# Performance work log

Hardware: AMD Instinct MI355X
Metric: run time of the kernel (lower is better)

Reference implementation:

```python
import jax, jax.numpy as jnp
from jax import lax
import numpy as np

B, T, EPROJS, DUNITS, ATT_DIM = 32, 2048, 1024, 1024, 1024
ACONV_CHANS, ACONV_FILTS = 10, 100
SCALING = 2.0


def setup_inputs() -> dict:
    key = jax.random.key(0)
    ks = jax.random.split(key, 12)
    s = 0.02
    return {
        "enc_hs_pad": jax.random.normal(ks[0], (B, T, EPROJS), jnp.float32),
        "enc_hs_len": jax.random.randint(ks[1], (B,), T // 2, T + 1, jnp.int32),
        "dec_z": jax.random.normal(ks[2], (B, DUNITS), jnp.float32),
        "att_prev": jax.random.uniform(ks[3], (B, T), jnp.float32) / T,
        "W_enc": jax.random.normal(ks[4], (EPROJS, ATT_DIM), jnp.float32) * s,
        "b_enc": jnp.zeros((ATT_DIM,), jnp.float32),
        "W_dec": jax.random.normal(ks[5], (DUNITS, ATT_DIM), jnp.float32) * s,
        "W_att": jax.random.normal(ks[6], (ACONV_CHANS, ATT_DIM), jnp.float32) * s,
        "conv_w": jax.random.normal(ks[7], (ACONV_CHANS, 1, 2 * ACONV_FILTS + 1), jnp.float32) * s,
        "gvec_w": jax.random.normal(ks[8], (ATT_DIM,), jnp.float32) * s,
        "gvec_b": jnp.zeros((), jnp.float32),
    }


def reference(enc_hs_pad, enc_hs_len, dec_z, att_prev, W_enc, b_enc, W_dec, W_att, conv_w, gvec_w, gvec_b):
    # location conv over previous attention: (B,1,T) -> (B,C,T), 'same' padding
    pad = (conv_w.shape[-1] - 1) // 2
    att_conv = lax.conv_general_dilated(
        att_prev[:, None, :], conv_w, window_strides=(1,),
        padding=[(pad, pad)], dimension_numbers=("NCH", "OIH", "NCH"))  # (B,C,T)
    loc = jnp.einsum("bct,cd->btd", att_conv, W_att)                     # mlp_att
    enc_proj = jnp.einsum("bte,ed->btd", enc_hs_pad, W_enc) + b_enc      # pre_compute_enc_h
    dec_proj = (dec_z @ W_dec)[:, None, :]                               # (B,1,D)
    e = jnp.tanh(loc + enc_proj + dec_proj) @ gvec_w + gvec_b            # (B,T)
    mask = jnp.arange(T)[None, :] >= enc_hs_len[:, None]                 # pad mask
    e = jnp.where(mask, -jnp.inf, e)
    w = jax.nn.softmax(SCALING * e, axis=1)                              # (B,T)
    c = jnp.einsum("bt,bte->be", w, enc_hs_pad)                          # weighted sum
    return c, w
```

## Files before the change

### kernel.cpp

```cpp
#include <hip/hip_runtime.h>
#include <hip/hip_bf16.h>
#include <math.h>

#define BB 32
#define TT 2048
#define EE 1024
#define DD 1024
#define MM (BB * TT)
#define CC 10
#define FW 201

typedef __attribute__((ext_vector_type(8))) short short8;
typedef __attribute__((ext_vector_type(4))) float f32x4;
typedef __attribute__((ext_vector_type(4))) float f4;
typedef __attribute__((ext_vector_type(8))) unsigned short u16x8;
typedef unsigned short u16;

__device__ __forceinline__ u16 f2bf(float f) {
  __hip_bfloat16 h = __float2bfloat16(f);
  return *reinterpret_cast<u16*>(&h);
}
__device__ __forceinline__ float bf2f(u16 u) {
  __hip_bfloat16 h;
  *reinterpret_cast<u16*>(&h) = u;
  return __bfloat162float(h);
}

__global__ void k_zero(float* __restrict__ e, float* __restrict__ c) {
  int i = blockIdx.x * 256 + threadIdx.x;
  e[i] = 0.f;
  if (i < BB * DD) c[i] = 0.f;
}

__global__ void k_cvt(const float* __restrict__ enc, u16* __restrict__ out) {
  long i = (long)blockIdx.x * 256 + threadIdx.x;
  const f4* ep = (const f4*)enc;
  f4 x = ep[2 * i], y = ep[2 * i + 1];
  u16x8 o;
  o[0] = f2bf(x[0]); o[1] = f2bf(x[1]); o[2] = f2bf(x[2]); o[3] = f2bf(x[3]);
  o[4] = f2bf(y[0]); o[5] = f2bf(y[1]); o[6] = f2bf(y[2]); o[7] = f2bf(y[3]);
  ((u16x8*)out)[i] = o;
}

__global__ void k_tw(const float* __restrict__ W, u16* __restrict__ Wt) {
  __shared__ float tile[64][65];
  int k0 = (blockIdx.x & 15) * 64;
  int n0 = (blockIdx.x >> 4) * 64;
  int tid = threadIdx.x;
  for (int i = tid; i < 4096; i += 256) {
    int r = i >> 6, cc = i & 63;
    tile[r][cc] = W[(k0 + r) * 1024 + n0 + cc];
  }
  __syncthreads();
  for (int i = tid; i < 4096; i += 256) {
    int nr = i >> 6, kc = i & 63;
    Wt[(n0 + nr) * 1024 + k0 + kc] = f2bf(tile[kc][nr]);
  }
}

__global__ void k_conv(const float* __restrict__ att_prev, const float* __restrict__ conv_w,
                       float* __restrict__ attc) {
  __shared__ float cw[CC * FW];
  __shared__ float ap[256 + 2 * 100];
  int b = blockIdx.x >> 3;
  int t0 = (blockIdx.x & 7) * 256;
  int tid = threadIdx.x;
  for (int i = tid; i < CC * FW; i += 256) cw[i] = conv_w[i];
  for (int i = tid; i < 456; i += 256) {
    int t = t0 - 100 + i;
    ap[i] = (t >= 0 && t < TT) ? att_prev[b * TT + t] : 0.f;
  }
  __syncthreads();
  float acc[CC];
#pragma unroll
  for (int c = 0; c < CC; ++c) acc[c] = 0.f;
  for (int f = 0; f < FW; ++f) {
    float x = ap[tid + f];
#pragma unroll
    for (int c = 0; c < CC; ++c) acc[c] += x * cw[c * FW + f];
  }
  int t = t0 + tid;
  float* o = attc + (size_t)(b * TT + t) * CC;
#pragma unroll
  for (int c = 0; c < CC; ++c) o[c] = acc[c];
}

__global__ void k_decp(const float* __restrict__ dec_z, const float* __restrict__ W_dec,
                       float* __restrict__ decp) {
  int b = blockIdx.x >> 2, dc = blockIdx.x & 3;
  __shared__ float z[1024];
  for (int i = threadIdx.x; i < 1024; i += 256) z[i] = dec_z[(b << 10) + i];
  __syncthreads();
  int d = (dc << 8) + threadIdx.x;
  float a0 = 0, a1 = 0, a2 = 0, a3 = 0;
  for (int k = 0; k < 1024; k += 4) {
    a0 += z[k + 0] * W_dec[(k + 0) * 1024 + d];
    a1 += z[k + 1] * W_dec[(k + 1) * 1024 + d];
    a2 += z[k + 2] * W_dec[(k + 2) * 1024 + d];
    a3 += z[k + 3] * W_dec[(k + 3) * 1024 + d];
  }
  decp[(b << 10) + d] = (a0 + a1) + (a2 + a3);
}

__global__ __launch_bounds__(256, 2) void k_gemm(
    const u16* __restrict__ A, const u16* __restrict__ Bt,
    const float* __restrict__ benc, const float* __restrict__ decp,
    const float* __restrict__ attc, const float* __restrict__ watt,
    const float* __restrict__ gvec, float* __restrict__ e) {
  __shared__ u16 sA[2][128 * 32];
  __shared__ u16 sB[2][128 * 32];
  __shared__ float s_col[128];
  __shared__ float s_g[128];
  __shared__ float s_watt[CC * 128];
  __shared__ float s_attc[128 * CC];
  __shared__ float s_ep[128][2];

  int tid = threadIdx.x;
  int w = tid >> 6, lane = tid & 63;
  int orig = ((blockIdx.x & 7) << 9) + (blockIdx.x >> 3);
  int bm = orig >> 3, bn = orig & 7;
  int brow = bm << 7;
  int bcol = bn << 7;
  int b = brow >> 11;

  if (tid < 128) {
    s_col[tid] = benc[bcol + tid] + decp[(b << 10) + bcol + tid];
    s_g[tid] = gvec[bcol + tid];
    s_ep[tid][0] = 0.f;
    s_ep[tid][1] = 0.f;
  }
  for (int i = tid; i < CC * 128; i += 256) {
    int c = i >> 7, d = i & 127;
    s_watt[c * 128 + d] = watt[c * 1024 + bcol + d];
  }
  for (int i = tid; i < 128 * CC; i += 256)
    s_attc[i] = attc[(size_t)brow * CC + i];

  f32x4 acc[4][4];
#pragma unroll
  for (int i = 0; i < 4; ++i)
#pragma unroll
    for (int j = 0; j < 4; ++j) acc[i][j] = (f32x4){0.f, 0.f, 0.f, 0.f};

  int wm = w >> 1, wn = w & 1;
  int frl = lane & 15, fkg = lane >> 4;

  auto stage = [&](int buf, int kt) {
    int k0 = kt << 5;
#pragma unroll
    for (int q = 0; q < 2; ++q) {
      int ci = (q << 8) + (w << 6) + lane;
      int row = ci >> 2, p = ci & 3;
      int kg = (p - (row >> 1)) & 3;
      const u16* ga = A + (size_t)(brow + row) * 1024 + k0 + (kg << 3);
      u16* la = &sA[buf][((q << 8) + (w << 6)) << 3];
      __builtin_amdgcn_global_load_lds(
          (const __attribute__((address_space(1))) void*)ga,
          (__attribute__((address_space(3))) void*)la, 16, 0, 0);
      const u16* gb = Bt + (size_t)(bcol + row) * 1024 + k0 + (kg << 3);
      u16* lb = &sB[buf][((q << 8) + (w << 6)) << 3];
      __builtin_amdgcn_global_load_lds(
          (const __attribute__((address_space(1))) void*)gb,
          (__attribute__((address_space(3))) void*)lb, 16, 0, 0);
    }
  };

  stage(0, 0);
  __syncthreads();

  for (int kt = 0; kt < 32; ++kt) {
    int cur = kt & 1;
    if (kt < 31) stage(cur ^ 1, kt + 1);
    short8 af[4], bfr[4];
#pragma unroll
    for (int mi = 0; mi < 4; ++mi) {
      int r = (wm << 6) + (mi << 4) + frl;
      int p = (fkg + (r >> 1)) & 3;
      af[mi] = *(const short8*)&sA[cur][(r << 5) + (p << 3)];
    }
#pragma unroll
    for (int ni = 0; ni < 4; ++ni) {
      int r = (wn << 6) + (ni << 4) + frl;
      int p = (fkg + (r >> 1)) & 3;
      bfr[ni] = *(const short8*)&sB[cur][(r << 5) + (p << 3)];
    }
#pragma unroll
    for (int mi = 0; mi < 4; ++mi)
#pragma unroll
      for (int ni = 0; ni < 4; ++ni)
        acc[mi][ni] = __builtin_amdgcn_mfma_f32_16x16x32_bf16(af[mi], bfr[ni], acc[mi][ni], 0, 0, 0);
    __syncthreads();
  }

#pragma unroll
  for (int mi = 0; mi < 4; ++mi) {
#pragma unroll
    for (int j = 0; j < 4; ++j) {
      int rl = (wm << 6) + (mi << 4) + (fkg << 2) + j;
      float ar[CC];
#pragma unroll
      for (int c = 0; c < CC; ++c) ar[c] = s_attc[rl * CC + c];
      float esum = 0.f;
#pragma unroll
      for (int ni = 0; ni < 4; ++ni) {
        int col = (wn << 6) + (ni << 4) + frl;
        float qv = acc[mi][ni][j] + s_col[col];
#pragma unroll
        for (int c = 0; c < CC; ++c) qv += ar[c] * s_watt[c * 128 + col];
        esum += s_g[col] * tanhf(qv);
      }
#pragma unroll
      for (int o = 8; o >= 1; o >>= 1) esum += __shfl_xor(esum, o, 16);
      if (frl == 0) s_ep[rl][wn] = esum;
    }
  }
  __syncthreads();
  if (tid < 128) atomicAdd(&e[brow + tid], s_ep[tid][0] + s_ep[tid][1]);
}

__global__ __launch_bounds__(256) void k_softmax(const float* __restrict__ e,
                                                 const int* __restrict__ len,
                                                 float* __restrict__ wout) {
  int b = blockIdx.x;
  int L = len[b];
  const float* eb = e + b * TT;
  __shared__ float red[4], red2[4];
  int tid = threadIdx.x, w = tid >> 6, lane = tid & 63;
  float m = -3.4e38f;
  for (int t = tid; t < TT; t += 256)
    if (t < L) m = fmaxf(m, eb[t]);
  for (int o = 32; o >= 1; o >>= 1) m = fmaxf(m, __shfl_xor(m, o, 64));
  if (lane == 0) red[w] = m;
  __syncthreads();
  m = fmaxf(fmaxf(red[0], red[1]), fmaxf(red[2], red[3]));
  float s = 0.f;
  for (int t = tid; t < TT; t += 256)
    if (t < L) s += __expf(2.f * (eb[t] - m));
  for (int o = 32; o >= 1; o >>= 1) s += __shfl_xor(s, o, 64);
  if (lane == 0) red2[w] = s;
  __syncthreads();
  s = red2[0] + red2[1] + red2[2] + red2[3];
  float inv = 1.f / s;
  for (int t = tid; t < TT; t += 256)
    wout[b * TT + t] = (t < L) ? __expf(2.f * (eb[t] - m)) * inv : 0.f;
}

__global__ __launch_bounds__(256) void k_ctx(const u16* __restrict__ encbf,
                                             const float* __restrict__ wout,
                                             float* __restrict__ c) {
  int bid = blockIdx.x;
  int b = bid >> 5;
  int ec = (bid >> 3) & 3;
  int tc = bid & 7;
  int col = (ec << 8) + threadIdx.x;
  const u16* eb = encbf + ((size_t)(b * TT + tc * 256) << 10) + col;
  const float* wb = wout + b * TT + tc * 256;
  float a0 = 0, a1 = 0, a2 = 0, a3 = 0;
  for (int t = 0; t < 256; t += 4) {
    a0 += wb[t + 0] * bf2f(eb[(size_t)(t + 0) << 10]);
    a1 += wb[t + 1] * bf2f(eb[(size_t)(t + 1) << 10]);
    a2 += wb[t + 2] * bf2f(eb[(size_t)(t + 2) << 10]);
    a3 += wb[t + 3] * bf2f(eb[(size_t)(t + 3) << 10]);
  }
  atomicAdd(&c[(b << 10) + col], (a0 + a1) + (a2 + a3));
}

extern "C" void kernel_launch(void* const* d_in, const int* in_sizes, int n_in,
                              void* d_out, int out_size, void* d_ws, size_t ws_size,
                              hipStream_t stream) {
  const float* enc = (const float*)d_in[0];
  const int* elen = (const int*)d_in[1];
  const float* dec_z = (const float*)d_in[2];
  const float* att_prev = (const float*)d_in[3];
  const float* W_enc = (const float*)d_in[4];
  const float* b_enc = (const float*)d_in[5];
  const float* W_dec = (const float*)d_in[6];
  const float* W_att = (const float*)d_in[7];
  const float* conv_w = (const float*)d_in[8];
  const float* gvec_w = (const float*)d_in[9];

  char* ws = (char*)d_ws;
  u16* encbf = (u16*)ws;  ws += (size_t)MM * EE * 2;
  u16* Wt = (u16*)ws;     ws += (size_t)EE * DD * 2;
  float* attc = (float*)ws; ws += (size_t)MM * CC * 4;
  float* decp = (float*)ws; ws += (size_t)BB * DD * 4;
  float* e = (float*)ws;    ws += (size_t)MM * 4;

  float* c = (float*)d_out;
  float* wout = c + BB * DD;

  k_zero<<<256, 256, 0, stream>>>(e, c);
  k_cvt<<<(MM * EE / 8) / 256, 256, 0, stream>>>(enc, encbf);
  k_tw<<<256, 256, 0, stream>>>(W_enc, Wt);
  k_conv<<<256, 256, 0, stream>>>(att_prev, conv_w, attc);
  k_decp<<<128, 256, 0, stream>>>(dec_z, W_dec, decp);
  k_gemm<<<4096, 256, 0, stream>>>(encbf, Wt, b_enc, decp, attc, W_att, gvec_w, e);
  k_softmax<<<BB, 256, 0, stream>>>(e, elen, wout);
  k_ctx<<<1024, 256, 0, stream>>>(encbf, wout, c);
}
```

Before: 732.5 us.

## Rewrite attention GEMM with 256x256 tiles, deep LDS pipeline, and vectorized context

The main GEMM moves from 128x128 tiles with 256 threads to 256x256 tiles with 512 threads and 128KB of dynamic LDS. Its K loop is a multi-stage global_load_lds pipeline with explicit vmcnt waits, barriers and setprio around the MFMA bursts. Per-column partial energies are written to four separate buffers and summed in softmax, so the atomics and the zeroing pass for e go away. tanhf is replaced by an exp/rcp approximation. The decoder projection is split along K across more blocks, and the context kernel uses 8-wide bf16 loads and skips zero weights. The larger tiles cut operand refetch, at the cost of higher register and LDS pressure, which could limit occupancy.

Measured after the change: 715.1 us. 1.02x faster.

```diff
diff --git a/kernel.cpp b/kernel.cpp
--- a/kernel.cpp
+++ b/kernel.cpp
@@ -25,11 +25,14 @@
   *reinterpret_cast<u16*>(&h) = u;
   return __bfloat162float(h);
 }
-
-__global__ void k_zero(float* __restrict__ e, float* __restrict__ c) {
+__device__ __forceinline__ float tanh_fast(float x) {
+  float ex = __expf(2.f * x);
+  return 1.f - 2.f * __builtin_amdgcn_rcpf(ex + 1.f);
+}
+
+__global__ void k_zero(float* __restrict__ c) {
   int i = blockIdx.x * 256 + threadIdx.x;
-  e[i] = 0.f;
-  if (i < BB * DD) c[i] = 0.f;
+  c[i] = 0.f;
 }
 
 __global__ void k_cvt(const float* __restrict__ enc, u16* __restrict__ out) {
@@ -85,184 +88,253 @@
   for (int c = 0; c < CC; ++c) o[c] = acc[c];
 }
 
-__global__ void k_decp(const float* __restrict__ dec_z, const float* __restrict__ W_dec,
-                       float* __restrict__ decp) {
-  int b = blockIdx.x >> 2, dc = blockIdx.x & 3;
+__global__ __launch_bounds__(256) void k_decp(const float* __restrict__ dec_z,
+                                              const float* __restrict__ W_dec,
+                                              float* __restrict__ decp) {
+  int b = blockIdx.x >> 4;
+  int c0 = (blockIdx.x & 15) << 6;
   __shared__ float z[1024];
+  __shared__ float red[4][64];
   for (int i = threadIdx.x; i < 1024; i += 256) z[i] = dec_z[(b << 10) + i];
   __syncthreads();
-  int d = (dc << 8) + threadIdx.x;
-  float a0 = 0, a1 = 0, a2 = 0, a3 = 0;
-  for (int k = 0; k < 1024; k += 4) {
-    a0 += z[k + 0] * W_dec[(k + 0) * 1024 + d];
-    a1 += z[k + 1] * W_dec[(k + 1) * 1024 + d];
-    a2 += z[k + 2] * W_dec[(k + 2) * 1024 + d];
-    a3 += z[k + 3] * W_dec[(k + 3) * 1024 + d];
-  }
-  decp[(b << 10) + d] = (a0 + a1) + (a2 + a3);
-}
-
-__global__ __launch_bounds__(256, 2) void k_gemm(
+  int d = c0 + (threadIdx.x & 63), ks = threadIdx.x >> 6;
+  float a = 0.f;
+  const float* Wp = W_dec + (size_t)(ks << 8) * 1024 + d;
+  const float* zp = z + (ks << 8);
+#pragma unroll 4
+  for (int k = 0; k < 256; ++k) a += zp[k] * Wp[(size_t)k * 1024];
+  red[ks][threadIdx.x & 63] = a;
+  __syncthreads();
+  if (threadIdx.x < 64)
+    decp[(b << 10) + c0 + threadIdx.x] =
+        (red[0][threadIdx.x] + red[1][threadIdx.x]) + (red[2][threadIdx.x] + red[3][threadIdx.x]);
+}
+
+#define VM8 asm volatile("s_waitcnt vmcnt(8)" ::: "memory")
+#define VM4 asm volatile("s_waitcnt vmcnt(4)" ::: "memory")
+#define VM0 asm volatile("s_waitcnt vmcnt(0)" ::: "memory")
+
+__global__ __launch_bounds__(512, 2) void k_gemm8(
     const u16* __restrict__ A, const u16* __restrict__ Bt,
     const float* __restrict__ benc, const float* __restrict__ decp,
     const float* __restrict__ attc, const float* __restrict__ watt,
-    const float* __restrict__ gvec, float* __restrict__ e) {
-  __shared__ u16 sA[2][128 * 32];
-  __shared__ u16 sB[2][128 * 32];
-  __shared__ float s_col[128];
-  __shared__ float s_g[128];
-  __shared__ float s_watt[CC * 128];
-  __shared__ float s_attc[128 * CC];
-  __shared__ float s_ep[128][2];
+    const float* __restrict__ gvec, float* __restrict__ epart) {
+  extern __shared__ u16 smem[];
+  u16* sA = smem;
+  u16* sB = smem + 32768;
 
   int tid = threadIdx.x;
-  int w = tid >> 6, lane = tid & 63;
-  int orig = ((blockIdx.x & 7) << 9) + (blockIdx.x >> 3);
-  int bm = orig >> 3, bn = orig & 7;
-  int brow = bm << 7;
-  int bcol = bn << 7;
+  int lane = tid & 63, wid = tid >> 6;
+  int frl = lane & 15, fkg = lane >> 4;
+  int wm = wid >> 2, wn = wid & 3;
+
+  int orig = (blockIdx.x & 7) * 128 + (blockIdx.x >> 3);
+  int bm = orig >> 2, bn = orig & 3;
+  int brow = bm << 8;
+  int bcol = bn << 8;
   int b = brow >> 11;
 
-  if (tid < 128) {
-    s_col[tid] = benc[bcol + tid] + decp[(b << 10) + bcol + tid];
-    s_g[tid] = gvec[bcol + tid];
-    s_ep[tid][0] = 0.f;
-    s_ep[tid][1] = 0.f;
-  }
-  for (int i = tid; i < CC * 128; i += 256) {
-    int c = i >> 7, d = i & 127;
-    s_watt[c * 128 + d] = watt[c * 1024 + bcol + d];
-  }
-  for (int i = tid; i < 128 * CC; i += 256)
-    s_attc[i] = attc[(size_t)brow * CC + i];
-
-  f32x4 acc[4][4];
-#pragma unroll
-  for (int i = 0; i < 4; ++i)
-#pragma unroll
-    for (int j = 0; j < 4; ++j) acc[i][j] = (f32x4){0.f, 0.f, 0.f, 0.f};
-
-  int wm = w >> 1, wn = w & 1;
-  int frl = lane & 15, fkg = lane >> 4;
-
-  auto stage = [&](int buf, int kt) {
-    int k0 = kt << 5;
+  auto stA = [&](int par, int kk, int tile) {
+    u16* region = sA + ((par * 2 + kk) << 13);
+    const u16* gb = A + (size_t)brow * 1024 + tile * 64 + kk * 32;
 #pragma unroll
     for (int q = 0; q < 2; ++q) {
-      int ci = (q << 8) + (w << 6) + lane;
-      int row = ci >> 2, p = ci & 3;
-      int kg = (p - (row >> 1)) & 3;
-      const u16* ga = A + (size_t)(brow + row) * 1024 + k0 + (kg << 3);
-      u16* la = &sA[buf][((q << 8) + (w << 6)) << 3];
+      int s = (q << 9) + tid;
+      int r = s >> 2, ch = s & 3;
+      int cs = ch ^ ((r >> 1) & 3);
+      const u16* src = gb + (size_t)r * 1024 + (cs << 3);
+      u16* dst = region + (((q << 9) + (tid & ~63)) << 3);
       __builtin_amdgcn_global_load_lds(
-          (const __attribute__((address_space(1))) void*)ga,
-          (__attribute__((address_space(3))) void*)la, 16, 0, 0);
-      const u16* gb = Bt + (size_t)(bcol + row) * 1024 + k0 + (kg << 3);
-      u16* lb = &sB[buf][((q << 8) + (w << 6)) << 3];
-      __builtin_amdgcn_global_load_lds(
-          (const __attribute__((address_space(1))) void*)gb,
-          (__attribute__((address_space(3))) void*)lb, 16, 0, 0);
+          (const __attribute__((address_space(1))) void*)src,
+          (__attribute__((address_space(3))) void*)dst, 16, 0, 0);
     }
   };
-
-  stage(0, 0);
-  __syncthreads();
-
-  for (int kt = 0; kt < 32; ++kt) {
-    int cur = kt & 1;
-    if (kt < 31) stage(cur ^ 1, kt + 1);
-    short8 af[4], bfr[4];
-#pragma unroll
-    for (int mi = 0; mi < 4; ++mi) {
-      int r = (wm << 6) + (mi << 4) + frl;
-      int p = (fkg + (r >> 1)) & 3;
-      af[mi] = *(const short8*)&sA[cur][(r << 5) + (p << 3)];
+  auto stB = [&](int par, int kk, int tile) {
+    u16* region = sB + ((par * 2 + kk) << 13);
+    const u16* gb = Bt + (size_t)bcol * 1024 + tile * 64 + kk * 32;
+#pragma unroll
+    for (int q = 0; q < 2; ++q) {
+      int s = (q << 9) + tid;
+      int r = s >> 2, ch = s & 3;
+      int cs = ch ^ ((r >> 1) & 3);
+      const u16* src = gb + (size_t)r * 1024 + (cs << 3);
+      u16* dst = region + (((q << 9) + (tid & ~63)) << 3);
+      __builtin_amdgcn_global_load_lds(
+          (const __attribute__((address_space(1))) void*)src,
+          (__attribute__((address_space(3))) void*)dst, 16, 0, 0);
     }
-#pragma unroll
-    for (int ni = 0; ni < 4; ++ni) {
-      int r = (wn << 6) + (ni << 4) + frl;
-      int p = (fkg + (r >> 1)) & 3;
-      bfr[ni] = *(const short8*)&sB[cur][(r << 5) + (p << 3)];
+  };
+  auto rdA = [&](int par, int kk, int mi) -> short8 {
+    int row = (wm << 7) + (mi << 4) + frl;
+    int g = fkg ^ ((row >> 1) & 3);
+    return *(const short8*)(sA + ((par * 2 + kk) << 13) + (row << 5) + (g << 3));
+  };
+  auto rdB = [&](int par, int kk, int ni) -> short8 {
+    int row = (wn << 6) + (ni << 4) + frl;
+    int g = fkg ^ ((row >> 1) & 3);
+    return *(const short8*)(sB + ((par * 2 + kk) << 13) + (row << 5) + (g << 3));
+  };
+
+  f32x4 acc[8][4];
+#pragma unroll
+  for (int i = 0; i < 8; ++i)
+#pragma unroll
+    for (int j = 0; j < 4; ++j) acc[i][j] = (f32x4){0.f, 0.f, 0.f, 0.f};
+  short8 afr[4], bfr[4];
+
+#define PH(PAR, KK, CH, STAGE, WAIT)                                          \
+  {                                                                           \
+    if ((CH) == 0) {                                                          \
+      _Pragma("unroll") for (int ni = 0; ni < 4; ++ni)                        \
+          bfr[ni] = rdB(PAR, KK, ni);                                         \
+    }                                                                         \
+    _Pragma("unroll") for (int i = 0; i < 4; ++i)                             \
+        afr[i] = rdA(PAR, KK, (CH)*4 + i);                                    \
+    STAGE;                                                                    \
+    WAIT;                                                                     \
+    __builtin_amdgcn_s_barrier();                                             \
+    __builtin_amdgcn_s_setprio(1);                                            \
+    _Pragma("unroll") for (int i = 0; i < 4; ++i)                             \
+        _Pragma("unroll") for (int ni = 0; ni < 4; ++ni)                      \
+            acc[(CH)*4 + i][ni] = __builtin_amdgcn_mfma_f32_16x16x32_bf16(    \
+                afr[i], bfr[ni], acc[(CH)*4 + i][ni], 0, 0, 0);               \
+    __builtin_amdgcn_s_setprio(0);                                            \
+    __builtin_amdgcn_s_barrier();                                             \
+  }
+
+  stA(0, 0, 0); stB(0, 0, 0);
+  stA(0, 1, 0); stB(0, 1, 0);
+  stA(1, 0, 1); stB(1, 0, 1);
+  VM8;
+  __builtin_amdgcn_s_barrier();
+
+#pragma unroll 1
+  for (int I = 0; I < 7; ++I) {
+    int t = 2 * I;
+    PH(0, 0, 0, stA(1, 1, t + 1), ((void)0));
+    PH(0, 0, 1, stB(1, 1, t + 1), VM8);
+    PH(0, 1, 0, stA(0, 0, t + 2), ((void)0));
+    PH(0, 1, 1, stB(0, 0, t + 2), VM8);
+    PH(1, 0, 0, stA(0, 1, t + 2), ((void)0));
+    PH(1, 0, 1, stB(0, 1, t + 2), VM8);
+    PH(1, 1, 0, stA(1, 0, t + 3), ((void)0));
+    PH(1, 1, 1, stB(1, 0, t + 3), VM8);
+  }
+  PH(0, 0, 0, stA(1, 1, 15), ((void)0));
+  PH(0, 0, 1, stB(1, 1, 15), VM8);
+  PH(0, 1, 0, ((void)0), ((void)0));
+  PH(0, 1, 1, ((void)0), VM4);
+  PH(1, 0, 0, ((void)0), ((void)0));
+  PH(1, 0, 1, ((void)0), VM0);
+  PH(1, 1, 0, ((void)0), ((void)0));
+  PH(1, 1, 1, ((void)0), ((void)0));
+#undef PH
+
+  __syncthreads();
+  float* fsm = (float*)smem;
+  float* se_attc = fsm;
+  float* se_watt = fsm + 2560;
+  float* se_col  = fsm + 5120;
+  float* se_g    = fsm + 5376;
+  float* se_ep   = fsm + 5632;
+  for (int i = tid; i < 2560; i += 512) {
+    se_attc[i] = attc[(size_t)brow * 10 + i];
+    se_watt[i] = watt[(i >> 8) * 1024 + bcol + (i & 255)];
+  }
+  if (tid < 256) {
+    se_col[tid] = benc[bcol + tid] + decp[(b << 10) + bcol + tid];
+    se_g[tid] = gvec[bcol + tid];
+  }
+  __syncthreads();
+
+#pragma unroll
+  for (int mi = 0; mi < 8; ++mi) {
+#pragma unroll
+    for (int j = 0; j < 4; ++j) {
+      int rl = (wm << 7) + (mi << 4) + (fkg << 2) + j;
+      float ar[CC];
+#pragma unroll
+      for (int c = 0; c < CC; ++c) ar[c] = se_attc[rl * 10 + c];
+      float esum = 0.f;
+#pragma unroll
+      for (int ni = 0; ni < 4; ++ni) {
+        int cl = (wn << 6) + (ni << 4) + frl;
+        float qv = acc[mi][ni][j] + se_col[cl];
+#pragma unroll
+        for (int c = 0; c < CC; ++c) qv += ar[c] * se_watt[c * 256 + cl];
+        esum += se_g[cl] * tanh_fast(qv);
+      }
+#pragma unroll
+      for (int o = 8; o >= 1; o >>= 1) esum += __shfl_xor(esum, o, 16);
+      if (frl == 0) se_ep[rl * 4 + wn] = esum;
     }
-#pragma unroll
-    for (int mi = 0; mi < 4; ++mi)
-#pragma unroll
-      for (int ni = 0; ni < 4; ++ni)
-        acc[mi][ni] = __builtin_amdgcn_mfma_f32_16x16x32_bf16(af[mi], bfr[ni], acc[mi][ni], 0, 0, 0);
-    __syncthreads();
-  }
-
-#pragma unroll
-  for (int mi = 0; mi < 4; ++mi) {
-#pragma unroll
-    for (int j = 0; j < 4; ++j) {
-      int rl = (wm << 6) + (mi << 4) + (fkg << 2) + j;
-      float ar[CC];
-#pragma unroll
-      for (int c = 0; c < CC; ++c) ar[c] = s_attc[rl * CC + c];
-      float esum = 0.f;
-#pragma unroll
-      for (int ni = 0; ni < 4; ++ni) {
-        int col = (wn << 6) + (ni << 4) + frl;
-        float qv = acc[mi][ni][j] + s_col[col];
-#pragma unroll
-        for (int c = 0; c < CC; ++c) qv += ar[c] * s_watt[c * 128 + col];
-        esum += s_g[col] * tanhf(qv);
-      }
-#pragma unroll
-      for (int o = 8; o >= 1; o >>= 1) esum += __shfl_xor(esum, o, 16);
-      if (frl == 0) s_ep[rl][wn] = esum;
-    }
-  }
-  __syncthreads();
-  if (tid < 128) atomicAdd(&e[brow + tid], s_ep[tid][0] + s_ep[tid][1]);
-}
-
-__global__ __launch_bounds__(256) void k_softmax(const float* __restrict__ e,
+  }
+  __syncthreads();
+  if (tid < 256)
+    epart[bn * MM + brow + tid] =
+        (se_ep[tid * 4 + 0] + se_ep[tid * 4 + 1]) + (se_ep[tid * 4 + 2] + se_ep[tid * 4 + 3]);
+}
+
+__global__ __launch_bounds__(256) void k_softmax(const float* __restrict__ ep,
                                                  const int* __restrict__ len,
                                                  float* __restrict__ wout) {
   int b = blockIdx.x;
   int L = len[b];
-  const float* eb = e + b * TT;
+  __shared__ float se[TT];
   __shared__ float red[4], red2[4];
   int tid = threadIdx.x, w = tid >> 6, lane = tid & 63;
-  float m = -3.4e38f;
+  for (int t = tid; t < TT; t += 256) {
+    int m = b * TT + t;
+    se[t] = (ep[m] + ep[MM + m]) + (ep[2 * MM + m] + ep[3 * MM + m]);
+  }
+  __syncthreads();
+  float mx = -3.4e38f;
   for (int t = tid; t < TT; t += 256)
-    if (t < L) m = fmaxf(m, eb[t]);
-  for (int o = 32; o >= 1; o >>= 1) m = fmaxf(m, __shfl_xor(m, o, 64));
-  if (lane == 0) red[w] = m;
-  __syncthreads();
-  m = fmaxf(fmaxf(red[0], red[1]), fmaxf(red[2], red[3]));
+    if (t < L) mx = fmaxf(mx, se[t]);
+  for (int o = 32; o >= 1; o >>= 1) mx = fmaxf(mx, __shfl_xor(mx, o, 64));
+  if (lane == 0) red[w] = mx;
+  __syncthreads();
+  mx = fmaxf(fmaxf(red[0], red[1]), fmaxf(red[2], red[3]));
   float s = 0.f;
   for (int t = tid; t < TT; t += 256)
-    if (t < L) s += __expf(2.f * (eb[t] - m));
+    if (t < L) s += __expf(2.f * (se[t] - mx));
   for (int o = 32; o >= 1; o >>= 1) s += __shfl_xor(s, o, 64);
   if (lane == 0) red2[w] = s;
   __syncthreads();
-  s = red2[0] + red2[1] + red2[2] + red2[3];
+  s = (red2[0] + red2[1]) + (red2[2] + red2[3]);
   float inv = 1.f / s;
   for (int t = tid; t < TT; t += 256)
-    wout[b * TT + t] = (t < L) ? __expf(2.f * (eb[t] - m)) * inv : 0.f;
+    wout[b * TT + t] = (t < L) ? __expf(2.f * (se[t] - mx)) * inv : 0.f;
 }
 
 __global__ __launch_bounds__(256) void k_ctx(const u16* __restrict__ encbf,
                                              const float* __restrict__ wout,
                                              float* __restrict__ c) {
-  int bid = blockIdx.x;
-  int b = bid >> 5;
-  int ec = (bid >> 3) & 3;
-  int tc = bid & 7;
-  int col = (ec << 8) + threadIdx.x;
-  const u16* eb = encbf + ((size_t)(b * TT + tc * 256) << 10) + col;
-  const float* wb = wout + b * TT + tc * 256;
-  float a0 = 0, a1 = 0, a2 = 0, a3 = 0;
-  for (int t = 0; t < 256; t += 4) {
-    a0 += wb[t + 0] * bf2f(eb[(size_t)(t + 0) << 10]);
-    a1 += wb[t + 1] * bf2f(eb[(size_t)(t + 1) << 10]);
-    a2 += wb[t + 2] * bf2f(eb[(size_t)(t + 2) << 10]);
-    a3 += wb[t + 3] * bf2f(eb[(size_t)(t + 3) << 10]);
-  }
-  atomicAdd(&c[(b << 10) + col], (a0 + a1) + (a2 + a3));
+  int b = blockIdx.x >> 3;
+  int t0 = (blockIdx.x & 7) << 8;
+  int col8 = (threadIdx.x & 127) << 3;
+  int rp = threadIdx.x >> 7;
+  const float* wb = wout + b * TT + t0;
+  float acc[8] = {0, 0, 0, 0, 0, 0, 0, 0};
+  for (int tt = rp; tt < 256; tt += 2) {
+    float wv = wb[tt];
+    if (wv == 0.f) continue;
+    u16x8 v = *(const u16x8*)(encbf + (((size_t)(b * TT + t0 + tt)) << 10) + col8);
+#pragma unroll
+    for (int j = 0; j < 8; ++j) acc[j] += wv * bf2f(v[j]);
+  }
+  __shared__ float red[128][8];
+  if (rp) {
+#pragma unroll
+    for (int j = 0; j < 8; ++j) red[threadIdx.x & 127][j] = acc[j];
+  }
+  __syncthreads();
+  if (!rp) {
+#pragma unroll
+    for (int j = 0; j < 8; ++j) acc[j] += red[threadIdx.x][j];
+#pragma unroll
+    for (int j = 0; j < 8; ++j) atomicAdd(&c[(b << 10) + col8 + j], acc[j]);
+  }
 }
 
 extern "C" void kernel_launch(void* const* d_in, const int* in_sizes, int n_in,
@@ -280,21 +352,24 @@
   const float* gvec_w = (const float*)d_in[9];
 
   char* ws = (char*)d_ws;
-  u16* encbf = (u16*)ws;  ws += (size_t)MM * EE * 2;
-  u16* Wt = (u16*)ws;     ws += (size_t)EE * DD * 2;
+  u16* encbf = (u16*)ws;    ws += (size_t)MM * EE * 2;
+  u16* Wt = (u16*)ws;       ws += (size_t)EE * DD * 2;
   float* attc = (float*)ws; ws += (size_t)MM * CC * 4;
   float* decp = (float*)ws; ws += (size_t)BB * DD * 4;
-  float* e = (float*)ws;    ws += (size_t)MM * 4;
+  float* ep = (float*)ws;   ws += (size_t)4 * MM * 4;
 
   float* c = (float*)d_out;
   float* wout = c + BB * DD;
 
-  k_zero<<<256, 256, 0, stream>>>(e, c);
+  hipFuncSetAttribute((const void*)k_gemm8,
+                      hipFuncAttributeMaxDynamicSharedMemorySize, 131072);
+
+  k_zero<<<128, 256, 0, stream>>>(c);
   k_cvt<<<(MM * EE / 8) / 256, 256, 0, stream>>>(enc, encbf);
   k_tw<<<256, 256, 0, stream>>>(W_enc, Wt);
   k_conv<<<256, 256, 0, stream>>>(att_prev, conv_w, attc);
-  k_decp<<<128, 256, 0, stream>>>(dec_z, W_dec, decp);
-  k_gemm<<<4096, 256, 0, stream>>>(encbf, Wt, b_enc, decp, attc, W_att, gvec_w, e);
-  k_softmax<<<BB, 256, 0, stream>>>(e, elen, wout);
-  k_ctx<<<1024, 256, 0, stream>>>(encbf, wout, c);
-}
+  k_decp<<<512, 256, 0, stream>>>(dec_z, W_dec, decp);
+  k_gemm8<<<1024, 512, 131072, stream>>>(encbf, Wt, b_enc, decp, attc, W_att, gvec_w, ep);
+  k_softmax<<<BB, 256, 0, stream>>>(ep, elen, wout);
+  k_ctx<<<256, 256, 0, stream>>>(encbf, wout, c);
+}
```
